# Kernel tuning notes

Measured on AMD Instinct MI355X. Metric: run time of the kernel, lower is better.

## Reference

```python
import jax, jax.numpy as jnp
import numpy as np

N_NODES = 100000
N_EDGES = 1600000
D_IN, D_HID, N_CLASSES = 128, 128, 64


def setup_inputs() -> dict:
    key = jax.random.key(0)
    k1, k2, k3, k4 = jax.random.split(key, 4)
    x = jax.random.normal(k1, (N_NODES, D_IN), dtype=jnp.float32)
    edge_index = jax.random.randint(k2, (2, N_EDGES), 0, N_NODES, dtype=jnp.int64)
    W1 = jax.random.normal(k3, (D_IN, D_HID), dtype=jnp.float32) * 0.05
    b1 = jnp.zeros((D_HID,), dtype=jnp.float32)
    W2 = jax.random.normal(k4, (D_HID, N_CLASSES), dtype=jnp.float32) * 0.05
    b2 = jnp.zeros((N_CLASSES,), dtype=jnp.float32)
    return {"x": x, "edge_index": edge_index, "W1": W1, "b1": b1, "W2": W2, "b2": b2}


def _gcn_layer(x, src_all, dst_all, edge_w, W, b):
    # PyG GCNConv: x' = D^{-1/2} (A + I) D^{-1/2} (x W) + b
    n = x.shape[0]
    h = x @ W                                   # [N, out]
    msg = h[src_all] * edge_w[:, None]          # [E+N, out]
    out = jax.ops.segment_sum(msg, dst_all, num_segments=n)
    return out + b


def reference(x, edge_index, W1, b1, W2, b2):
    n = x.shape[0]
    src, dst = edge_index[0], edge_index[1]
    loop = jnp.arange(n, dtype=src.dtype)
    src_all = jnp.concatenate([src, loop])      # self-loops added (GCNConv default)
    dst_all = jnp.concatenate([dst, loop])
    deg = jax.ops.segment_sum(jnp.ones_like(dst_all, dtype=x.dtype), dst_all,
                              num_segments=n)
    dinv = jnp.where(deg > 0, jax.lax.rsqrt(deg), 0.0)
    edge_w = dinv[src_all] * dinv[dst_all]      # symmetric normalization

    h = _gcn_layer(x, src_all, dst_all, edge_w, W1, b1)
    h = jax.nn.relu(h)                          # dropout is identity in eval mode
    h = _gcn_layer(h, src_all, dst_all, edge_w, W2, b2)
    return jax.nn.log_softmax(h, axis=1)
```

## Files before the change

kernel.cpp:

```cpp
#include <hip/hip_runtime.h>
#include <math.h>

#define DIN 128
#define NCLS 64
#define BCAP 5120
#define SCALE1 64.0f
#define SCALE2 256.0f

typedef __attribute__((ext_vector_type(4))) float  f32x4;
typedef __attribute__((ext_vector_type(2))) float  f32x2;
typedef __attribute__((ext_vector_type(8))) short  bf16x8;

__device__ inline unsigned short f2bf(float f) {
    unsigned int u = __float_as_uint(f);
    u += 0x7fff + ((u >> 16) & 1);
    return (unsigned short)(u >> 16);
}


__global__ __launch_bounds__(256) void binA_k(const int* __restrict__ ei,
                                              int* __restrict__ gcnt,
                                              unsigned int* __restrict__ tmp,
                                              int E, int NB) {
    __shared__ int lcnt[512];
    __shared__ int gpos[512];
    const int t = threadIdx.x;
    for (int i = t; i < NB; i += 256) lcnt[i] = 0;
    __syncthreads();

    const int base = blockIdx.x * 4096;
    unsigned int pk[16];
    short bk[16], rk[16];
#pragma unroll
    for (int k = 0; k < 16; ++k) {
        int e = base + k * 256 + t;
        if (e < E) {
            int s = ei[e];
            int d = ei[E + e];
            int b = d >> 8;
            pk[k] = ((unsigned int)s << 8) | (unsigned int)(d & 255);
            bk[k] = (short)b;
            rk[k] = (short)atomicAdd(&lcnt[b], 1);
        } else {
            bk[k] = -1;
        }
    }
    __syncthreads();
    for (int i = t; i < NB; i += 256)
        gpos[i] = lcnt[i] ? atomicAdd(&gcnt[i], lcnt[i]) : 0;
    __syncthreads();
#pragma unroll
    for (int k = 0; k < 16; ++k) {
        if (bk[k] >= 0) {
            int b = bk[k];
            int pos = gpos[b] + rk[k];
            if (pos < BCAP) tmp[(size_t)b * BCAP + pos] = pk[k];
        }
    }
}

__global__ __launch_bounds__(512) void scanb_k(const int* __restrict__ gcnt,
                                               int* __restrict__ bbase, int NB) {
    __shared__ int tmp[512];
    int t = threadIdx.x;
    int v = (t < NB) ? gcnt[t] : 0;
    tmp[t] = v; __syncthreads();
    for (int o = 1; o < 512; o <<= 1) {
        int x = (t >= o) ? tmp[t - o] : 0;
        __syncthreads();
        tmp[t] += x;
        __syncthreads();
    }
    if (t < NB) bbase[t] = (t == 0) ? 0 : tmp[t - 1];
}

__global__ __launch_bounds__(256) void binB_k(const unsigned int* __restrict__ tmp,
                                              const int* __restrict__ gcnt,
                                              const int* __restrict__ bbase,
                                              int* __restrict__ off,
                                              float* __restrict__ dinv,
                                              int* __restrict__ srcs,
                                              int N, int E) {
    __shared__ unsigned int stg[BCAP];
    __shared__ int lcnt[256], sc[256], loff[256], lcur[256];
    const int b = blockIdx.x, t = threadIdx.x;
    int cnt = gcnt[b];
    if (cnt > BCAP) cnt = BCAP;
    const int base = bbase[b];
    lcnt[t] = 0; lcur[t] = 0;
    __syncthreads();
    for (int i = t; i < cnt; i += 256) {
        unsigned int v = tmp[(size_t)b * BCAP + i];
        stg[i] = v;
        atomicAdd(&lcnt[v & 255u], 1);
    }
    __syncthreads();
    sc[t] = lcnt[t]; __syncthreads();
    for (int o = 1; o < 256; o <<= 1) {
        int x = (t >= o) ? sc[t - o] : 0;
        __syncthreads();
        sc[t] += x;
        __syncthreads();
    }
    int excl = (t == 0) ? 0 : sc[t - 1];
    loff[t] = excl;
    int node = b * 256 + t;
    if (node <= N) off[node] = base + excl;
    if (node < N)  dinv[node] = rsqrtf(1.0f + (float)lcnt[t]);
    __syncthreads();
    for (int i = t; i < cnt; i += 256) {
        unsigned int v = stg[i];
        int l = v & 255u;
        int r = atomicAdd(&lcur[l], 1);
        srcs[base + loff[l] + r] = (int)(v >> 8);
    }
}


__global__ void wprep_k(const float* __restrict__ W1, const float* __restrict__ W2,
                        unsigned short* __restrict__ wt1, unsigned short* __restrict__ wt2,
                        int* __restrict__ gcnt, int NB) {
    int i = blockIdx.x * 256 + threadIdx.x;
    if (i < 128 * 128) { int k = i >> 7, n = i & 127; wt1[n * 128 + k] = f2bf(W1[i]); }
    if (i < 128 * 64)  { int k = i >> 6, n = i & 63;  wt2[n * 128 + k] = f2bf(W2[i]); }
    if (i < NB)        gcnt[i] = 0;
}


__global__ __launch_bounds__(256) void mgemm_k(const float* __restrict__ A,
                                               const unsigned short* __restrict__ Bt,
                                               const float* __restrict__ dinv,
                                               unsigned char* __restrict__ C,
                                               float oscale, int N) {
    constexpr int LDK = DIN + 8;
    constexpr int BN  = 128;
    __shared__ unsigned short As[64 * LDK];
    __shared__ unsigned short Bs[BN * LDK];
    const int tid  = threadIdx.x;
    const int row0 = blockIdx.x * 64;

    for (int idx = tid; idx < BN * 16; idx += 256) {
        int n = idx >> 4, c = (idx & 15) << 3;
        *(uint4*)&Bs[n * LDK + c] = *(const uint4*)&Bt[n * DIN + c];
    }
    for (int idx = tid; idx < 64 * 16; idx += 256) {
        int r = idx >> 4, c = (idx & 15) << 3;
        int gr = row0 + r;
        unsigned short v[8];
        if (gr < N) {
            f32x4 a0 = *(const f32x4*)&A[(size_t)gr * DIN + c];
            f32x4 a1 = *(const f32x4*)&A[(size_t)gr * DIN + c + 4];
            v[0] = f2bf(a0.x); v[1] = f2bf(a0.y); v[2] = f2bf(a0.z); v[3] = f2bf(a0.w);
            v[4] = f2bf(a1.x); v[5] = f2bf(a1.y); v[6] = f2bf(a1.z); v[7] = f2bf(a1.w);
        } else {
#pragma unroll
            for (int j = 0; j < 8; ++j) v[j] = 0;
        }
        *(uint4*)&As[r * LDK + c] = *(const uint4*)v;
    }
    __syncthreads();

    const int wave = tid >> 6, lane = tid & 63;
    const int lrow = lane & 15, kq = lane >> 4;
    constexpr int NT = BN / 16;
    f32x4 acc[NT];
#pragma unroll
    for (int t = 0; t < NT; ++t) acc[t] = (f32x4){0.f, 0.f, 0.f, 0.f};

    const unsigned short* Abase = &As[(wave * 16 + lrow) * LDK + kq * 8];
    const unsigned short* Bbase = &Bs[lrow * LDK + kq * 8];
#pragma unroll
    for (int kk = 0; kk < 4; ++kk) {
        bf16x8 a = *(const bf16x8*)(Abase + kk * 32);
#pragma unroll
        for (int t = 0; t < NT; ++t) {
            bf16x8 b = *(const bf16x8*)(Bbase + t * 16 * LDK + kk * 32);
            acc[t] = __builtin_amdgcn_mfma_f32_16x16x32_bf16(a, b, acc[t], 0, 0, 0);
        }
    }

    const int rb = row0 + wave * 16 + kq * 4;
#pragma unroll
    for (int r = 0; r < 4; ++r) {
        int gr = rb + r;
        if (gr < N) {
            float sc2 = dinv[gr] * oscale;
#pragma unroll
            for (int t = 0; t < NT; t += 2) {
                int pk = __builtin_amdgcn_cvt_pk_fp8_f32(acc[t][r] * sc2,
                                                         acc[t + 1][r] * sc2, 0, false);
                C[(size_t)gr * BN + t * 16 + lrow]       = (unsigned char)(pk & 0xff);
                C[(size_t)gr * BN + (t + 1) * 16 + lrow] = (unsigned char)((pk >> 8) & 0xff);
            }
        }
    }
}

__device__ inline void dec8(uint2 v, f32x2& x0, f32x2& x1, f32x2& x2, f32x2& x3) {
    x0 += __builtin_amdgcn_cvt_pk_f32_fp8((int)v.x, false);
    x1 += __builtin_amdgcn_cvt_pk_f32_fp8((int)v.x, true);
    x2 += __builtin_amdgcn_cvt_pk_f32_fp8((int)v.y, false);
    x3 += __builtin_amdgcn_cvt_pk_f32_fp8((int)v.y, true);
}

__device__ inline void dec16(uint4 v, f32x2& x0, f32x2& x1, f32x2& x2, f32x2& x3,
                             f32x2& x4, f32x2& x5, f32x2& x6, f32x2& x7) {
    x0 += __builtin_amdgcn_cvt_pk_f32_fp8((int)v.x, false);
    x1 += __builtin_amdgcn_cvt_pk_f32_fp8((int)v.x, true);
    x2 += __builtin_amdgcn_cvt_pk_f32_fp8((int)v.y, false);
    x3 += __builtin_amdgcn_cvt_pk_f32_fp8((int)v.y, true);
    x4 += __builtin_amdgcn_cvt_pk_f32_fp8((int)v.z, false);
    x5 += __builtin_amdgcn_cvt_pk_f32_fp8((int)v.z, true);
    x6 += __builtin_amdgcn_cvt_pk_f32_fp8((int)v.w, false);
    x7 += __builtin_amdgcn_cvt_pk_f32_fp8((int)v.w, true);
}


__global__ __launch_bounds__(512, 8) void fuse2_k(const unsigned char* __restrict__ hs,
                                                  const int* __restrict__ off,
                                                  const int* __restrict__ srcs,
                                                  const float* __restrict__ dinv,
                                                  const float* __restrict__ b1,
                                                  const unsigned short* __restrict__ Bt,
                                                  unsigned char* __restrict__ C,
                                                  int N) {
    constexpr int LDK = DIN + 8;
    __shared__ unsigned short As[64 * LDK];
    __shared__ unsigned short Bs[NCLS * LDK];
    const int tid  = threadIdx.x;
    const int row0 = blockIdx.x * 64;

    for (int idx = tid; idx < NCLS * 16; idx += 512) {
        int n = idx >> 4, c = (idx & 15) << 3;
        *(uint4*)&Bs[n * LDK + c] = *(const uint4*)&Bt[n * DIN + c];
    }

    const int oc = tid >> 3;
    const int sl = tid & 7;
    const int node = row0 + oc;
    const uint4* hp = (const uint4*)hs;

    if (node < N) {
        const int beg = off[node], end = off[node + 1];
        f32x2 a0={0.f,0.f},a1={0.f,0.f},a2={0.f,0.f},a3={0.f,0.f};
        f32x2 a4={0.f,0.f},a5={0.f,0.f},a6={0.f,0.f},a7={0.f,0.f};
        int i = beg;
        for (; i + 3 < end; i += 4) {
            unsigned s0 = (unsigned)srcs[i],     s1 = (unsigned)srcs[i + 1];
            unsigned s2 = (unsigned)srcs[i + 2], s3 = (unsigned)srcs[i + 3];
            uint4 v0 = hp[s0 * 8u + sl];
            uint4 v1 = hp[s1 * 8u + sl];
            uint4 v2 = hp[s2 * 8u + sl];
            uint4 v3 = hp[s3 * 8u + sl];
            dec16(v0, a0,a1,a2,a3,a4,a5,a6,a7);
            dec16(v1, a0,a1,a2,a3,a4,a5,a6,a7);
            dec16(v2, a0,a1,a2,a3,a4,a5,a6,a7);
            dec16(v3, a0,a1,a2,a3,a4,a5,a6,a7);
        }
        for (; i < end; ++i) {
            uint4 v = hp[(unsigned)srcs[i] * 8u + sl];
            dec16(v, a0,a1,a2,a3,a4,a5,a6,a7);
        }
        {
            uint4 v = hp[(unsigned)node * 8u + sl];
            dec16(v, a0,a1,a2,a3,a4,a5,a6,a7);
        }
        const float d = dinv[node] * (1.0f / SCALE1);
        const float4 w0 = ((const float4*)b1)[sl * 4 + 0];
        const float4 w1 = ((const float4*)b1)[sl * 4 + 1];
        const float4 w2 = ((const float4*)b1)[sl * 4 + 2];
        const float4 w3 = ((const float4*)b1)[sl * 4 + 3];
        float o0  = fmaxf(fmaf(d, a0.x, w0.x), 0.f);
        float o1  = fmaxf(fmaf(d, a0.y, w0.y), 0.f);
        float o2  = fmaxf(fmaf(d, a1.x, w0.z), 0.f);
        float o3  = fmaxf(fmaf(d, a1.y, w0.w), 0.f);
        float o4  = fmaxf(fmaf(d, a2.x, w1.x), 0.f);
        float o5  = fmaxf(fmaf(d, a2.y, w1.y), 0.f);
        float o6  = fmaxf(fmaf(d, a3.x, w1.z), 0.f);
        float o7  = fmaxf(fmaf(d, a3.y, w1.w), 0.f);
        float o8  = fmaxf(fmaf(d, a4.x, w2.x), 0.f);
        float o9  = fmaxf(fmaf(d, a4.y, w2.y), 0.f);
        float o10 = fmaxf(fmaf(d, a5.x, w2.z), 0.f);
        float o11 = fmaxf(fmaf(d, a5.y, w2.w), 0.f);
        float o12 = fmaxf(fmaf(d, a6.x, w3.x), 0.f);
        float o13 = fmaxf(fmaf(d, a6.y, w3.y), 0.f);
        float o14 = fmaxf(fmaf(d, a7.x, w3.z), 0.f);
        float o15 = fmaxf(fmaf(d, a7.y, w3.w), 0.f);
        uint4 u0, u1;
        u0.x = (unsigned)f2bf(o0)  | ((unsigned)f2bf(o1)  << 16);
        u0.y = (unsigned)f2bf(o2)  | ((unsigned)f2bf(o3)  << 16);
        u0.z = (unsigned)f2bf(o4)  | ((unsigned)f2bf(o5)  << 16);
        u0.w = (unsigned)f2bf(o6)  | ((unsigned)f2bf(o7)  << 16);
        u1.x = (unsigned)f2bf(o8)  | ((unsigned)f2bf(o9)  << 16);
        u1.y = (unsigned)f2bf(o10) | ((unsigned)f2bf(o11) << 16);
        u1.z = (unsigned)f2bf(o12) | ((unsigned)f2bf(o13) << 16);
        u1.w = (unsigned)f2bf(o14) | ((unsigned)f2bf(o15) << 16);
        *(uint4*)&As[oc * LDK + sl * 16]     = u0;
        *(uint4*)&As[oc * LDK + sl * 16 + 8] = u1;
    } else {
        uint4 z = make_uint4(0, 0, 0, 0);
        *(uint4*)&As[oc * LDK + sl * 16]     = z;
        *(uint4*)&As[oc * LDK + sl * 16 + 8] = z;
    }
    __syncthreads();

    const int wave = tid >> 6, lane = tid & 63;
    const int ws = wave & 3;
    const int ch = wave >> 2;
    const int lrow = lane & 15, kq = lane >> 4;
    f32x4 acc0 = (f32x4){0.f,0.f,0.f,0.f};
    f32x4 acc1 = (f32x4){0.f,0.f,0.f,0.f};

    const unsigned short* Abase = &As[(ws * 16 + lrow) * LDK + kq * 8];
    const unsigned short* Bbase = &Bs[(ch * 32 + lrow) * LDK + kq * 8];
#pragma unroll
    for (int kk = 0; kk < 4; ++kk) {
        bf16x8 a  = *(const bf16x8*)(Abase + kk * 32);
        bf16x8 b0 = *(const bf16x8*)(Bbase + kk * 32);
        bf16x8 b1v= *(const bf16x8*)(Bbase + 16 * LDK + kk * 32);
        acc0 = __builtin_amdgcn_mfma_f32_16x16x32_bf16(a, b0,  acc0, 0, 0, 0);
        acc1 = __builtin_amdgcn_mfma_f32_16x16x32_bf16(a, b1v, acc1, 0, 0, 0);
    }

    const int rb = row0 + ws * 16 + kq * 4;
#pragma unroll
    for (int r = 0; r < 4; ++r) {
        int gr = rb + r;
        if (gr < N) {
            float sc2 = dinv[gr] * SCALE2;
            int pk = __builtin_amdgcn_cvt_pk_fp8_f32(acc0[r] * sc2, acc1[r] * sc2, 0, false);
            C[(size_t)gr * NCLS + ch * 32 + lrow]      = (unsigned char)(pk & 0xff);
            C[(size_t)gr * NCLS + ch * 32 + 16 + lrow] = (unsigned char)((pk >> 8) & 0xff);
        }
    }
}


__global__ __launch_bounds__(256) void gather2_k(const unsigned char* __restrict__ hs,
                                                 const int* __restrict__ off,
                                                 const int* __restrict__ srcs,
                                                 const float* __restrict__ dinv,
                                                 const float* __restrict__ b2,
                                                 float* __restrict__ out, int N) {
    const int lane = threadIdx.x & 63;
    const int wave = threadIdx.x >> 6;
    const int o8 = lane >> 3;
    const int sl = lane & 7;
    const int node = blockIdx.x * 32 + wave * 8 + o8;
    if (node >= N) return;
    const int beg = off[node], end = off[node + 1];
    const uint2* hp = (const uint2*)hs;
    f32x2 A0 = {0.f,0.f}, A1 = {0.f,0.f}, A2 = {0.f,0.f}, A3 = {0.f,0.f};
    f32x2 C0 = {0.f,0.f}, C1 = {0.f,0.f}, C2 = {0.f,0.f}, C3 = {0.f,0.f};
    int i = beg;
    for (; i + 7 < end; i += 8) {
        unsigned s0 = (unsigned)srcs[i],     s1 = (unsigned)srcs[i + 1];
        unsigned s2 = (unsigned)srcs[i + 2], s3 = (unsigned)srcs[i + 3];
        unsigned s4 = (unsigned)srcs[i + 4], s5 = (unsigned)srcs[i + 5];
        unsigned s6 = (unsigned)srcs[i + 6], s7 = (unsigned)srcs[i + 7];
        uint2 v0 = hp[s0 * 8u + sl];
        uint2 v1 = hp[s1 * 8u + sl];
        uint2 v2 = hp[s2 * 8u + sl];
        uint2 v3 = hp[s3 * 8u + sl];
        uint2 v4 = hp[s4 * 8u + sl];
        uint2 v5 = hp[s5 * 8u + sl];
        uint2 v6 = hp[s6 * 8u + sl];
        uint2 v7 = hp[s7 * 8u + sl];
        dec8(v0, A0, A1, A2, A3);
        dec8(v1, C0, C1, C2, C3);
        dec8(v2, A0, A1, A2, A3);
        dec8(v3, C0, C1, C2, C3);
        dec8(v4, A0, A1, A2, A3);
        dec8(v5, C0, C1, C2, C3);
        dec8(v6, A0, A1, A2, A3);
        dec8(v7, C0, C1, C2, C3);
    }
    for (; i + 3 < end; i += 4) {
        unsigned s0 = (unsigned)srcs[i],     s1 = (unsigned)srcs[i + 1];
        unsigned s2 = (unsigned)srcs[i + 2], s3 = (unsigned)srcs[i + 3];
        uint2 v0 = hp[s0 * 8u + sl];
        uint2 v1 = hp[s1 * 8u + sl];
        uint2 v2 = hp[s2 * 8u + sl];
        uint2 v3 = hp[s3 * 8u + sl];
        dec8(v0, A0, A1, A2, A3);
        dec8(v1, C0, C1, C2, C3);
        dec8(v2, A0, A1, A2, A3);
        dec8(v3, C0, C1, C2, C3);
    }
    for (; i < end; ++i) {
        uint2 v = hp[(unsigned)srcs[i] * 8u + sl];
        dec8(v, A0, A1, A2, A3);
    }
    {
        uint2 v = hp[(unsigned)node * 8u + sl];
        dec8(v, C0, C1, C2, C3);
    }
    A0 += C0; A1 += C1; A2 += C2; A3 += C3;

    float d = dinv[node] * (1.0f / SCALE2);
    float4 ba = ((const float4*)b2)[sl * 2];
    float4 bb = ((const float4*)b2)[sl * 2 + 1];
    float v0 = fmaf(d, A0.x, ba.x);
    float v1 = fmaf(d, A0.y, ba.y);
    float v2 = fmaf(d, A1.x, ba.z);
    float v3 = fmaf(d, A1.y, ba.w);
    float v4 = fmaf(d, A2.x, bb.x);
    float v5 = fmaf(d, A2.y, bb.y);
    float v6 = fmaf(d, A3.x, bb.z);
    float v7 = fmaf(d, A3.y, bb.w);
    float m = fmaxf(fmaxf(fmaxf(v0, v1), fmaxf(v2, v3)), fmaxf(fmaxf(v4, v5), fmaxf(v6, v7)));
#pragma unroll
    for (int mk = 1; mk <= 4; mk <<= 1) m = fmaxf(m, __shfl_xor(m, mk, 64));
    float s = __expf(v0 - m) + __expf(v1 - m) + __expf(v2 - m) + __expf(v3 - m)
            + __expf(v4 - m) + __expf(v5 - m) + __expf(v6 - m) + __expf(v7 - m);
#pragma unroll
    for (int mk = 1; mk <= 4; mk <<= 1) s += __shfl_xor(s, mk, 64);
    float ls = m + __logf(s);
    float4 oa, ob;
    oa.x = v0 - ls; oa.y = v1 - ls; oa.z = v2 - ls; oa.w = v3 - ls;
    ob.x = v4 - ls; ob.y = v5 - ls; ob.z = v6 - ls; ob.w = v7 - ls;
    ((float4*)out)[(unsigned)node * 16u + sl * 2]     = oa;
    ((float4*)out)[(unsigned)node * 16u + sl * 2 + 1] = ob;
}


extern "C" void kernel_launch(void* const* d_in, const int* in_sizes, int n_in,
                              void* d_out, int out_size, void* d_ws, size_t ws_size,
                              hipStream_t stream) {
    const float* x  = (const float*)d_in[0];
    const int*   ei = (const int*)d_in[1];
    const float* W1 = (const float*)d_in[2];
    const float* b1 = (const float*)d_in[3];
    const float* W2 = (const float*)d_in[4];
    const float* b2 = (const float*)d_in[5];
    float* out = (float*)d_out;

    const int N  = in_sizes[0] / DIN;
    const int E  = in_sizes[1] / 2;
    const int NB = (N + 255) >> 8;

    char* p = (char*)d_ws;
    auto alloc = [&](size_t bytes) { void* r = p; p += (bytes + 255) & ~(size_t)255; return r; };
    float* dinv  = (float*)alloc((size_t)N * 4);
    int*   gcnt  = (int*)  alloc((size_t)NB * 4);
    int*   bbase = (int*)  alloc((size_t)NB * 4);
    int*   off   = (int*)  alloc((size_t)(N + 1) * 4);
    int*   srcs  = (int*)  alloc((size_t)E * 4);
    unsigned int* tmp = (unsigned int*)alloc((size_t)NB * BCAP * 4);
    unsigned short* wt1 = (unsigned short*)alloc(128 * 128 * 2);
    unsigned short* wt2 = (unsigned short*)alloc(64 * 128 * 2);
    unsigned char*  hs1 = (unsigned char*)alloc((size_t)N * DIN);
    unsigned char*  hs2 = (unsigned char*)alloc((size_t)N * NCLS);

    wprep_k<<<64, 256, 0, stream>>>(W1, W2, wt1, wt2, gcnt, NB);
    binA_k<<<(E + 4095) / 4096, 256, 0, stream>>>(ei, gcnt, tmp, E, NB);
    scanb_k<<<1, 512, 0, stream>>>(gcnt, bbase, NB);
    binB_k<<<NB, 256, 0, stream>>>(tmp, gcnt, bbase, off, dinv, srcs, N, E);

    mgemm_k<<<(N + 63) / 64, 256, 0, stream>>>(x, wt1, dinv, hs1, SCALE1, N);
    fuse2_k<<<(N + 63) / 64, 512, 0, stream>>>(hs1, off, srcs, dinv, b1, wt2, hs2, N);
    gather2_k<<<(N + 31) / 32, 256, 0, stream>>>(hs2, off, srcs, dinv, b2, out, N);
}
```

Before: 213.7 us.

## Replace two-pass bucket CSR build with degree-count, scan, and atomic scatter fused into GEMM launch

The CSR construction changes from a two-level bucketed binning scheme to a global degree count with per-node atomics, a three-kernel prefix scan, and an atomic-cursor scatter of source indices. The scatter blocks share one launch with the first-layer GEMM blocks so the two independent jobs can overlap. The dinv array is dropped and each consumer recomputes rsqrt from the degree. In exchange it adds more kernel launches, heavy global atomic contention, and neighbour order that is no longer deterministic, which may hurt gather locality.

Result: slower. 407.3 us (+90.6%).

```diff
diff --git a/kernel.cpp b/kernel.cpp
--- a/kernel.cpp
+++ b/kernel.cpp
@@ -3,7 +3,6 @@
 
 #define DIN 128
 #define NCLS 64
-#define BCAP 5120
 #define SCALE1 64.0f
 #define SCALE2 256.0f
 
@@ -18,126 +17,105 @@
 }
 
 
-__global__ __launch_bounds__(256) void binA_k(const int* __restrict__ ei,
-                                              int* __restrict__ gcnt,
-                                              unsigned int* __restrict__ tmp,
-                                              int E, int NB) {
-    __shared__ int lcnt[512];
-    __shared__ int gpos[512];
-    const int t = threadIdx.x;
-    for (int i = t; i < NB; i += 256) lcnt[i] = 0;
-    __syncthreads();
-
-    const int base = blockIdx.x * 4096;
-    unsigned int pk[16];
-    short bk[16], rk[16];
-#pragma unroll
-    for (int k = 0; k < 16; ++k) {
-        int e = base + k * 256 + t;
-        if (e < E) {
-            int s = ei[e];
-            int d = ei[E + e];
-            int b = d >> 8;
-            pk[k] = ((unsigned int)s << 8) | (unsigned int)(d & 255);
-            bk[k] = (short)b;
-            rk[k] = (short)atomicAdd(&lcnt[b], 1);
-        } else {
-            bk[k] = -1;
-        }
-    }
-    __syncthreads();
-    for (int i = t; i < NB; i += 256)
-        gpos[i] = lcnt[i] ? atomicAdd(&gcnt[i], lcnt[i]) : 0;
-    __syncthreads();
-#pragma unroll
-    for (int k = 0; k < 16; ++k) {
-        if (bk[k] >= 0) {
-            int b = bk[k];
-            int pos = gpos[b] + rk[k];
-            if (pos < BCAP) tmp[(size_t)b * BCAP + pos] = pk[k];
-        }
-    }
-}
-
-__global__ __launch_bounds__(512) void scanb_k(const int* __restrict__ gcnt,
-                                               int* __restrict__ bbase, int NB) {
-    __shared__ int tmp[512];
-    int t = threadIdx.x;
-    int v = (t < NB) ? gcnt[t] : 0;
+__global__ __launch_bounds__(256) void wprep_k(const float* __restrict__ W1,
+                                               const float* __restrict__ W2,
+                                               unsigned short* __restrict__ wt1,
+                                               unsigned short* __restrict__ wt2,
+                                               int* __restrict__ deg, int N) {
+    int i = blockIdx.x * 256 + threadIdx.x;
+    if (i < 128 * 128) { int k = i >> 7, n = i & 127; wt1[n * 128 + k] = f2bf(W1[i]); }
+    if (i < 128 * 64)  { int k = i >> 6, n = i & 63;  wt2[n * 128 + k] = f2bf(W2[i]); }
+    if (i < N)         deg[i] = 0;
+}
+
+
+__global__ __launch_bounds__(256) void degA_k(const int* __restrict__ ei,
+                                              int* __restrict__ deg, int E) {
+    int base = blockIdx.x * 2048 + threadIdx.x;
+#pragma unroll
+    for (int k = 0; k < 8; ++k) {
+        int e = base + k * 256;
+        if (e < E) atomicAdd(&deg[ei[E + e]], 1);
+    }
+}
+
+__global__ __launch_bounds__(1024) void scan1_k(const int* __restrict__ deg,
+                                                int* __restrict__ sinc,
+                                                int* __restrict__ btot, int N) {
+    __shared__ int tmp[1024];
+    int t = threadIdx.x, i = blockIdx.x * 1024 + t;
+    int v = (i < N) ? deg[i] : 0;
     tmp[t] = v; __syncthreads();
-    for (int o = 1; o < 512; o <<= 1) {
+    for (int o = 1; o < 1024; o <<= 1) {
         int x = (t >= o) ? tmp[t - o] : 0;
         __syncthreads();
         tmp[t] += x;
         __syncthreads();
     }
-    if (t < NB) bbase[t] = (t == 0) ? 0 : tmp[t - 1];
-}
-
-__global__ __launch_bounds__(256) void binB_k(const unsigned int* __restrict__ tmp,
-                                              const int* __restrict__ gcnt,
-                                              const int* __restrict__ bbase,
-                                              int* __restrict__ off,
-                                              float* __restrict__ dinv,
-                                              int* __restrict__ srcs,
-                                              int N, int E) {
-    __shared__ unsigned int stg[BCAP];
-    __shared__ int lcnt[256], sc[256], loff[256], lcur[256];
-    const int b = blockIdx.x, t = threadIdx.x;
-    int cnt = gcnt[b];
-    if (cnt > BCAP) cnt = BCAP;
-    const int base = bbase[b];
-    lcnt[t] = 0; lcur[t] = 0;
-    __syncthreads();
-    for (int i = t; i < cnt; i += 256) {
-        unsigned int v = tmp[(size_t)b * BCAP + i];
-        stg[i] = v;
-        atomicAdd(&lcnt[v & 255u], 1);
-    }
-    __syncthreads();
-    sc[t] = lcnt[t]; __syncthreads();
-    for (int o = 1; o < 256; o <<= 1) {
-        int x = (t >= o) ? sc[t - o] : 0;
+    if (i < N) sinc[i] = tmp[t];
+    if (t == 1023) btot[blockIdx.x] = tmp[1023];
+}
+
+__global__ __launch_bounds__(128) void scan2_k(const int* __restrict__ btot,
+                                               int* __restrict__ bex, int NB1) {
+    __shared__ int tmp[128];
+    int t = threadIdx.x;
+    int v = (t < NB1) ? btot[t] : 0;
+    tmp[t] = v; __syncthreads();
+    for (int o = 1; o < 128; o <<= 1) {
+        int x = (t >= o) ? tmp[t - o] : 0;
         __syncthreads();
-        sc[t] += x;
+        tmp[t] += x;
         __syncthreads();
     }
-    int excl = (t == 0) ? 0 : sc[t - 1];
-    loff[t] = excl;
-    int node = b * 256 + t;
-    if (node <= N) off[node] = base + excl;
-    if (node < N)  dinv[node] = rsqrtf(1.0f + (float)lcnt[t]);
-    __syncthreads();
-    for (int i = t; i < cnt; i += 256) {
-        unsigned int v = stg[i];
-        int l = v & 255u;
-        int r = atomicAdd(&lcur[l], 1);
-        srcs[base + loff[l] + r] = (int)(v >> 8);
-    }
-}
-
-
-__global__ void wprep_k(const float* __restrict__ W1, const float* __restrict__ W2,
-                        unsigned short* __restrict__ wt1, unsigned short* __restrict__ wt2,
-                        int* __restrict__ gcnt, int NB) {
-    int i = blockIdx.x * 256 + threadIdx.x;
-    if (i < 128 * 128) { int k = i >> 7, n = i & 127; wt1[n * 128 + k] = f2bf(W1[i]); }
-    if (i < 128 * 64)  { int k = i >> 6, n = i & 63;  wt2[n * 128 + k] = f2bf(W2[i]); }
-    if (i < NB)        gcnt[i] = 0;
-}
-
-
-__global__ __launch_bounds__(256) void mgemm_k(const float* __restrict__ A,
-                                               const unsigned short* __restrict__ Bt,
-                                               const float* __restrict__ dinv,
-                                               unsigned char* __restrict__ C,
-                                               float oscale, int N) {
+    if (t < NB1) bex[t] = tmp[t] - v;
+}
+
+__global__ __launch_bounds__(1024) void scan3_k(const int* __restrict__ deg,
+                                                const int* __restrict__ sinc,
+                                                const int* __restrict__ bex,
+                                                int* __restrict__ off,
+                                                int* __restrict__ cur, int N, int E) {
+    int t = threadIdx.x, i = blockIdx.x * 1024 + t;
+    if (i < N) {
+        int ex = sinc[i] - deg[i] + bex[blockIdx.x];
+        off[i] = ex;
+        cur[i] = ex;
+    }
+    if (i == N) off[N] = E;
+}
+
+
+__global__ __launch_bounds__(256) void smix_k(const int* __restrict__ ei,
+                                              int* __restrict__ cur,
+                                              int* __restrict__ srcs, int E,
+                                              const float* __restrict__ A,
+                                              const unsigned short* __restrict__ Bt,
+                                              const int* __restrict__ deg,
+                                              unsigned char* __restrict__ C,
+                                              float oscale, int N, int NS) {
     constexpr int LDK = DIN + 8;
     constexpr int BN  = 128;
     __shared__ unsigned short As[64 * LDK];
     __shared__ unsigned short Bs[BN * LDK];
+
+    if ((int)blockIdx.x < NS) {
+        int base = blockIdx.x * 2048 + threadIdx.x;
+#pragma unroll
+        for (int k = 0; k < 8; ++k) {
+            int e = base + k * 256;
+            if (e < E) {
+                int s = ei[e];
+                int d = ei[E + e];
+                int r = atomicAdd(&cur[d], 1);
+                srcs[r] = s;
+            }
+        }
+        return;
+    }
+
     const int tid  = threadIdx.x;
-    const int row0 = blockIdx.x * 64;
+    const int row0 = ((int)blockIdx.x - NS) * 64;
 
     for (int idx = tid; idx < BN * 16; idx += 256) {
         int n = idx >> 4, c = (idx & 15) << 3;
@@ -184,7 +162,7 @@
     for (int r = 0; r < 4; ++r) {
         int gr = rb + r;
         if (gr < N) {
-            float sc2 = dinv[gr] * oscale;
+            float sc2 = rsqrtf(1.0f + (float)deg[gr]) * oscale;
 #pragma unroll
             for (int t = 0; t < NT; t += 2) {
                 int pk = __builtin_amdgcn_cvt_pk_fp8_f32(acc[t][r] * sc2,
@@ -219,7 +197,7 @@
 __global__ __launch_bounds__(512, 8) void fuse2_k(const unsigned char* __restrict__ hs,
                                                   const int* __restrict__ off,
                                                   const int* __restrict__ srcs,
-                                                  const float* __restrict__ dinv,
+                                                  const int* __restrict__ deg,
                                                   const float* __restrict__ b1,
                                                   const unsigned short* __restrict__ Bt,
                                                   unsigned char* __restrict__ C,
@@ -265,7 +243,7 @@
             uint4 v = hp[(unsigned)node * 8u + sl];
             dec16(v, a0,a1,a2,a3,a4,a5,a6,a7);
         }
-        const float d = dinv[node] * (1.0f / SCALE1);
+        const float d = rsqrtf(1.0f + (float)deg[node]) * (1.0f / SCALE1);
         const float4 w0 = ((const float4*)b1)[sl * 4 + 0];
         const float4 w1 = ((const float4*)b1)[sl * 4 + 1];
         const float4 w2 = ((const float4*)b1)[sl * 4 + 2];
@@ -327,7 +305,7 @@
     for (int r = 0; r < 4; ++r) {
         int gr = rb + r;
         if (gr < N) {
-            float sc2 = dinv[gr] * SCALE2;
+            float sc2 = rsqrtf(1.0f + (float)deg[gr]) * SCALE2;
             int pk = __builtin_amdgcn_cvt_pk_fp8_f32(acc0[r] * sc2, acc1[r] * sc2, 0, false);
             C[(size_t)gr * NCLS + ch * 32 + lrow]      = (unsigned char)(pk & 0xff);
             C[(size_t)gr * NCLS + ch * 32 + 16 + lrow] = (unsigned char)((pk >> 8) & 0xff);
@@ -339,7 +317,7 @@
 __global__ __launch_bounds__(256) void gather2_k(const unsigned char* __restrict__ hs,
                                                  const int* __restrict__ off,
                                                  const int* __restrict__ srcs,
-                                                 const float* __restrict__ dinv,
+                                                 const int* __restrict__ deg,
                                                  const float* __restrict__ b2,
                                                  float* __restrict__ out, int N) {
     const int lane = threadIdx.x & 63;
@@ -397,7 +375,7 @@
     }
     A0 += C0; A1 += C1; A2 += C2; A3 += C3;
 
-    float d = dinv[node] * (1.0f / SCALE2);
+    float d = rsqrtf(1.0f + (float)deg[node]) * (1.0f / SCALE2);
     float4 ba = ((const float4*)b2)[sl * 2];
     float4 bb = ((const float4*)b2)[sl * 2 + 1];
     float v0 = fmaf(d, A0.x, ba.x);
@@ -435,29 +413,32 @@
     const float* b2 = (const float*)d_in[5];
     float* out = (float*)d_out;
 
-    const int N  = in_sizes[0] / DIN;
-    const int E  = in_sizes[1] / 2;
-    const int NB = (N + 255) >> 8;
+    const int N   = in_sizes[0] / DIN;
+    const int E   = in_sizes[1] / 2;
+    const int NB1 = (N + 1023) / 1024;
+    const int NS  = (E + 2047) / 2048;
+    const int NG  = (N + 63) / 64;
 
     char* p = (char*)d_ws;
     auto alloc = [&](size_t bytes) { void* r = p; p += (bytes + 255) & ~(size_t)255; return r; };
-    float* dinv  = (float*)alloc((size_t)N * 4);
-    int*   gcnt  = (int*)  alloc((size_t)NB * 4);
-    int*   bbase = (int*)  alloc((size_t)NB * 4);
-    int*   off   = (int*)  alloc((size_t)(N + 1) * 4);
-    int*   srcs  = (int*)  alloc((size_t)E * 4);
-    unsigned int* tmp = (unsigned int*)alloc((size_t)NB * BCAP * 4);
+    int* deg   = (int*)alloc((size_t)N * 4);
+    int* off   = (int*)alloc((size_t)(N + 1) * 4);
+    int* cur   = (int*)alloc((size_t)N * 4);
+    int* srcs  = (int*)alloc((size_t)E * 4);
+    int* sinc  = (int*)alloc((size_t)N * 4);
+    int* btot  = (int*)alloc(256 * 4);
+    int* bex   = (int*)alloc(256 * 4);
     unsigned short* wt1 = (unsigned short*)alloc(128 * 128 * 2);
     unsigned short* wt2 = (unsigned short*)alloc(64 * 128 * 2);
     unsigned char*  hs1 = (unsigned char*)alloc((size_t)N * DIN);
     unsigned char*  hs2 = (unsigned char*)alloc((size_t)N * NCLS);
 
-    wprep_k<<<64, 256, 0, stream>>>(W1, W2, wt1, wt2, gcnt, NB);
-    binA_k<<<(E + 4095) / 4096, 256, 0, stream>>>(ei, gcnt, tmp, E, NB);
-    scanb_k<<<1, 512, 0, stream>>>(gcnt, bbase, NB);
-    binB_k<<<NB, 256, 0, stream>>>(tmp, gcnt, bbase, off, dinv, srcs, N, E);
-
-    mgemm_k<<<(N + 63) / 64, 256, 0, stream>>>(x, wt1, dinv, hs1, SCALE1, N);
-    fuse2_k<<<(N + 63) / 64, 512, 0, stream>>>(hs1, off, srcs, dinv, b1, wt2, hs2, N);
-    gather2_k<<<(N + 31) / 32, 256, 0, stream>>>(hs2, off, srcs, dinv, b2, out, N);
-}
+    wprep_k<<<(N + 255) / 256, 256, 0, stream>>>(W1, W2, wt1, wt2, deg, N);
+    degA_k<<<NS, 256, 0, stream>>>(ei, deg, E);
+    scan1_k<<<NB1, 1024, 0, stream>>>(deg, sinc, btot, N);
+    scan2_k<<<1, 128, 0, stream>>>(btot, bex, NB1);
+    scan3_k<<<NB1, 1024, 0, stream>>>(deg, sinc, bex, off, cur, N, E);
+    smix_k<<<NS + NG, 256, 0, stream>>>(ei, cur, srcs, E, x, wt1, deg, hs1, SCALE1, N, NS);
+    fuse2_k<<<(N + 63) / 64, 512, 0, stream>>>(hs1, off, srcs, deg, b1, wt2, hs2, N);
+    gather2_k<<<(N + 31) / 32, 256, 0, stream>>>(hs2, off, srcs, deg, b2, out, N);
+}
```
